# Performance work log

Hardware: AMD Instinct MI355X
Metric: run time of the kernel (lower is better)

Reference implementation:

```python
import jax, jax.numpy as jnp
import numpy as np
from jax import lax

B, T = 64, 200
NUM_C, DIM_S, SIZE_M = 2000, 128, 50


def setup_inputs() -> dict:
    key = jax.random.key(0)
    ks = jax.random.split(key, 12)
    d = {}
    d['skill'] = jax.random.randint(ks[0], (B, T), 0, NUM_C)
    d['answer'] = jax.random.randint(ks[1], (B, T), 0, 2)
    s = 1.0 / np.sqrt(DIM_S)
    d['k_emb'] = jax.random.normal(ks[2], (NUM_C + 1, DIM_S), jnp.float32)
    d['v_emb'] = jax.random.normal(ks[3], (2 * NUM_C + 1, DIM_S), jnp.float32)
    # kaiming_normal on [size_m, dim_s]: std = sqrt(2/dim_s)
    d['Mk'] = jax.random.normal(ks[4], (SIZE_M, DIM_S), jnp.float32) * np.sqrt(2.0 / DIM_S)
    d['Mv0'] = jax.random.normal(ks[5], (SIZE_M, DIM_S), jnp.float32) * np.sqrt(2.0 / DIM_S)
    d['f_W'] = jax.random.normal(ks[6], (DIM_S, 2 * DIM_S), jnp.float32) * (1.0 / np.sqrt(2 * DIM_S))
    d['f_b'] = jnp.zeros((DIM_S,), jnp.float32)
    d['p_W'] = jax.random.normal(ks[7], (NUM_C, DIM_S), jnp.float32) * s
    d['p_b'] = jnp.zeros((NUM_C,), jnp.float32)
    d['e_W'] = jax.random.normal(ks[8], (DIM_S, DIM_S), jnp.float32) * s
    d['e_b'] = jnp.zeros((DIM_S,), jnp.float32)
    d['a_W'] = jax.random.normal(ks[9], (DIM_S, DIM_S), jnp.float32) * s
    d['a_b'] = jnp.zeros((DIM_S,), jnp.float32)
    return d


def reference(skill, answer, k_emb, v_emb, Mk, Mv0, f_W, f_b, p_W, p_b, e_W, e_b, a_W, a_b):
    num_c = p_W.shape[0]
    bsz = skill.shape[0]
    answer_x = jnp.where(answer == 2, 1, answer)
    x = skill + num_c * answer_x                       # [B,T]
    k = k_emb[skill]                                   # [B,T,D]
    v = v_emb[x]                                       # [B,T,D]
    w = jax.nn.softmax(jnp.einsum('btd,md->btm', k, Mk), axis=-1)   # [B,T,M]
    e = jax.nn.sigmoid(jnp.einsum('btd,ed->bte', v, e_W) + e_b)      # [B,T,D]
    a = jnp.tanh(jnp.einsum('btd,ed->bte', v, a_W) + a_b)            # [B,T,D]

    Mv_init = jnp.broadcast_to(Mv0, (bsz,) + Mv0.shape)              # [B,M,D]

    def step(Mvt, inp):
        et, at, wt = inp                               # [B,D],[B,D],[B,M]
        # read uses pre-update memory (Mv[:, :-1] in the torch code)
        read = jnp.einsum('bm,bmd->bd', wt, Mvt)
        Mvt_new = Mvt * (1.0 - wt[:, :, None] * et[:, None, :]) + wt[:, :, None] * at[:, None, :]
        return Mvt_new, read

    _, reads = lax.scan(step, Mv_init,
                        (e.transpose(1, 0, 2), a.transpose(1, 0, 2), w.transpose(1, 0, 2)))
    reads = reads.transpose(1, 0, 2)                   # [B,T,D]

    f = jnp.tanh(jnp.concatenate([reads, k], axis=-1) @ f_W.T + f_b)  # [B,T,D]
    p = jax.nn.sigmoid(f @ p_W.T + p_b)                # [B,T,num_c] (dropout is identity at eval)
    p = p[:, :-1, :]
    next_skill = skill[:, 1:]                          # [B,T-1]
    idx = jnp.minimum(next_skill, num_c - 1)
    pred = jnp.take_along_axis(p, idx[..., None], axis=-1)[..., 0]
    pred = jnp.where(next_skill < num_c, pred, 0.0)    # index num_c -> zero row in torch one_hot
    return pred
```

## Files before the change

kernel.cpp:

```cpp
#include <hip/hip_runtime.h>
#include <math.h>

#define Bsz 64
#define Tn 200
#define NUMC 2000
#define DS 128
#define SM 50
#define NTOK (Bsz*Tn)

typedef __attribute__((ext_vector_type(8))) short bfrag;
typedef __attribute__((ext_vector_type(4))) float f32x4;
typedef __attribute__((ext_vector_type(4))) unsigned int u32x4;

__device__ __forceinline__ unsigned short f2bf(float x) {
    unsigned int u = __builtin_bit_cast(unsigned int, x);
    u = u + 0x7fffu + ((u >> 16) & 1u);
    return (unsigned short)(u >> 16);
}
__device__ __forceinline__ unsigned int pack2(float a, float b) {
    return (unsigned int)f2bf(a) | ((unsigned int)f2bf(b) << 16);
}
__device__ __forceinline__ bfrag mk_frag(f32x4 x, f32x4 y) {
    u32x4 t;
    t[0] = pack2(x[0], x[1]); t[1] = pack2(x[2], x[3]);
    t[2] = pack2(y[0], y[1]); t[3] = pack2(y[2], y[3]);
    return __builtin_bit_cast(bfrag, t);
}

__device__ __forceinline__ float fast_exp(float x)  { return __builtin_amdgcn_exp2f(x * 1.44269504f); }
__device__ __forceinline__ float fast_rcp(float x)  { return __builtin_amdgcn_rcpf(x); }
__device__ __forceinline__ float fast_sigmoid(float x) { return fast_rcp(1.f + fast_exp(-x)); }
__device__ __forceinline__ float fast_tanh(float x) { return 1.f - 2.f * fast_rcp(fast_exp(2.f * x) + 1.f); }

__global__ __launch_bounds__(256) void k0_cast(
    const float* __restrict__ eW, const float* __restrict__ aW,
    const float* __restrict__ fW, const float* __restrict__ Mk,
    unsigned int* __restrict__ BeaU, unsigned int* __restrict__ BkmU,
    unsigned int* __restrict__ Bf0U)
{
    const int g = blockIdx.x * 256 + threadIdx.x;
    if (g >= 9216) return;
    int gm, mat;
    unsigned int* dst;
    if (g < 4096)      { mat = 0; gm = g;        dst = BeaU; }
    else if (g < 7168) { mat = 1; gm = g - 4096; dst = BkmU; }
    else               { mat = 2; gm = g - 7168; dst = Bf0U; }
    const int nt = gm >> 8, r = gm & 255, ki = r >> 6, L = r & 63;
    const int n = nt * 16 + (L & 15);
    const int k = ki * 32 + (L >> 4) * 8;

    const float* src = nullptr;
    if (mat == 0) {
        src = (n < 128) ? (eW + (size_t)n * DS + k) : (aW + (size_t)(n - 128) * DS + k);
    } else if (mat == 1) {
        if (n < 128)      src = fW + (size_t)n * (2 * DS) + DS + k;
        else if (n < 128 + SM) src = Mk + (size_t)(n - 128) * DS + k;
    } else {
        src = fW + (size_t)n * (2 * DS) + k;
    }
    float v[8];
    #pragma unroll
    for (int j = 0; j < 8; j++) v[j] = src ? src[j] : 0.f;
    u32x4 o;
    o[0] = pack2(v[0], v[1]); o[1] = pack2(v[2], v[3]);
    o[2] = pack2(v[4], v[5]); o[3] = pack2(v[6], v[7]);
    ((u32x4*)dst)[gm] = o;
}

__global__ __launch_bounds__(64, 4) void k1_gemm(
    const int* __restrict__ skill, const int* __restrict__ answer,
    const float* __restrict__ k_emb, const float* __restrict__ v_emb,
    const unsigned int* __restrict__ BeaU, const unsigned int* __restrict__ BkmU,
    const float* __restrict__ eB, const float* __restrict__ aB,
    float* __restrict__ w2, float* __restrict__ e_buf,
    float* __restrict__ a_buf, float* __restrict__ kp_buf)
{
    const int bid = blockIdx.x;
    const int tile = bid / 7, role = bid % 7;
    const int L = threadIdx.x, L15 = L & 15, quad = L >> 4;
    const int tok0 = tile * 16;
    const int tokA = tok0 + L15;
    const int row0 = tok0 + quad * 4;

    const int s = skill[tokA];
    const float* ap;
    if (role < 4) {
        const int an = answer[tokA];
        const int ax = (an == 2) ? 1 : an;
        ap = v_emb + ((size_t)(s + NUMC * ax)) * DS + quad * 8;
    } else {
        ap = k_emb + (size_t)s * DS + quad * 8;
    }
    bfrag Af[4];
    #pragma unroll
    for (int ki = 0; ki < 4; ki++) {
        const f32x4* a4 = (const f32x4*)(ap + ki * 32);
        Af[ki] = mk_frag(a4[0], a4[1]);
    }

    const bfrag* Bp = (role < 4) ? (const bfrag*)BeaU : (const bfrag*)BkmU;
    const int g0 = (role < 4) ? role * 4 : (role - 4) * 4;

    f32x4 acc[4];
    #pragma unroll
    for (int t = 0; t < 4; t++) acc[t] = (f32x4){0.f,0.f,0.f,0.f};

    #pragma unroll
    for (int half = 0; half < 2; half++) {
        bfrag bh[2][4];
        #pragma unroll
        for (int tt = 0; tt < 2; tt++)
            #pragma unroll
            for (int ki = 0; ki < 4; ki++)
                bh[tt][ki] = Bp[(size_t)((g0 + half * 2 + tt) * 4 + ki) * 64 + L];
        #pragma unroll
        for (int ki = 0; ki < 4; ki++)
            #pragma unroll
            for (int tt = 0; tt < 2; tt++)
                acc[half * 2 + tt] = __builtin_amdgcn_mfma_f32_16x16x32_bf16(
                    Af[ki], bh[tt][ki], acc[half * 2 + tt], 0, 0, 0);
    }

    if (role == 6) {
        #pragma unroll
        for (int reg = 0; reg < 4; reg++) {
            float mx = -1e30f;
            #pragma unroll
            for (int t = 0; t < 4; t++) { const int c = t * 16 + L15; if (c < SM) mx = fmaxf(mx, acc[t][reg]); }
            #pragma unroll
            for (int msk = 1; msk <= 8; msk <<= 1) mx = fmaxf(mx, __shfl_xor(mx, msk));
            float ex[4]; float ssum = 0.f;
            #pragma unroll
            for (int t = 0; t < 4; t++) {
                const int c = t * 16 + L15;
                ex[t] = (c < SM) ? fast_exp(acc[t][reg] - mx) : 0.f;
                ssum += ex[t];
            }
            #pragma unroll
            for (int msk = 1; msk <= 8; msk <<= 1) ssum += __shfl_xor(ssum, msk);
            const float inv = fast_rcp(ssum);
            float* wp = w2 + (size_t)(row0 + reg) * 64;
            #pragma unroll
            for (int t = 0; t < 4; t++) {
                const int c = t * 16 + L15;
                const int idx = (c < 13) ? c
                              : (c < 26) ? c + 3
                              : (c < 39) ? c + 6
                              : (c < 50) ? c + 9
                              : (c < 53) ? c - 37
                              : (c < 56) ? c - 24
                              : (c < 59) ? c - 11
                              : c;
                wp[idx] = ex[t] * inv;
            }
        }
    } else {
        const int nb = (role & 1) * 64;
        float* obuf = (role < 2) ? e_buf : (role < 4) ? a_buf : kp_buf;
        const float* bias = (role < 2) ? eB : aB;
        #pragma unroll
        for (int t = 0; t < 4; t++) {
            const int n = nb + t * 16 + L15;
            const float bv = (role < 4) ? bias[n] : 0.f;
            #pragma unroll
            for (int reg = 0; reg < 4; reg++) {
                float v = acc[t][reg] + bv;
                if (role < 2)      v = fast_sigmoid(v);
                else if (role < 4) v = fast_tanh(v);
                obuf[(size_t)(row0 + reg) * DS + n] = v;
            }
        }
    }
}

__global__ __launch_bounds__(64) void k2_scan(
    const float* __restrict__ w2, const float* __restrict__ e_buf,
    const float* __restrict__ a_buf, const float* __restrict__ Mv0,
    unsigned short* __restrict__ reads)
{
    const int bid  = blockIdx.x;
    const int b    = bid >> 3;
    const int dseg = bid & 7;
    const int lane = threadIdx.x;
    const int mg   = lane >> 4;
    const int dd   = lane & 15;
    const int d    = dseg * 16 + dd;
    const int mstart = mg * 13;
    const int gcol = mg * 16;
    const int base = b * Tn;

    float Mv[13];
    #pragma unroll
    for (int j = 0; j < 13; j++) {
        const int m = (mstart + j < SM) ? (mstart + j) : (SM - 1);
        Mv[j] = Mv0[(size_t)m * DS + d];
    }

    float ev[2][4], av[2][4], wd[2][4];
    f32x4 wa[2][4], wb[2][4], wc[2][4];

    #define LOADS(S, T0)                                                       \
        { _Pragma("unroll")                                                    \
          for (int i_ = 0; i_ < 4; i_++) {                                     \
              const int t_ = (T0) + i_;                                        \
              const int tc_ = (t_ < Tn) ? t_ : 0;                              \
              ev[S][i_] = e_buf[(size_t)(base + tc_) * DS + d];                \
              av[S][i_] = a_buf[(size_t)(base + tc_) * DS + d];                \
              const float* wp_ = w2 + (size_t)(base + tc_) * 64 + gcol;        \
              wa[S][i_] = *(const f32x4*)wp_;                                  \
              wb[S][i_] = *(const f32x4*)(wp_ + 4);                            \
              wc[S][i_] = *(const f32x4*)(wp_ + 8);                            \
              wd[S][i_] = wp_[12];                                             \
          } }

    #define PROC4(S, T0)                                                       \
        { float r4[4];                                                         \
          _Pragma("unroll")                                                    \
          for (int it = 0; it < 4; it++) {                                     \
              const float ev_ = ev[S][it], av_ = av[S][it];                    \
              float rd = 0.f;                                                  \
              _Pragma("unroll")                                                \
              for (int j = 0; j < 13; j++) {                                   \
                  const float wm = (j < 4) ? wa[S][it][j]                      \
                                 : (j < 8) ? wb[S][it][j - 4]                  \
                                 : (j < 12) ? wc[S][it][j - 8]                 \
                                 : wd[S][it];                                  \
                  rd = fmaf(wm, Mv[j], rd);                        \
                  Mv[j] = fmaf(-wm, fmaf(ev_, Mv[j], -av_), Mv[j]);            \
              }                                                                \
              rd += __shfl_xor(rd, 16);                                        \
              rd += __shfl_xor(rd, 32);                                        \
              r4[it] = rd;                                                     \
          }                                                                    \
          const float val = (mg == 0) ? r4[0] : (mg == 1) ? r4[1]              \
                          : (mg == 2) ? r4[2] : r4[3];                         \
          reads[(size_t)(base + (T0) + mg) * DS + d] = f2bf(val); }

    LOADS(0, 0) LOADS(1, 4)

    for (int blk = 0; blk < 25; blk++) {
        const int t0 = blk * 8;
        PROC4(0, t0)     LOADS(0, t0 + 8)
        PROC4(1, t0 + 4) LOADS(1, t0 + 12)
    }
    #undef LOADS
    #undef PROC4
}

__global__ __launch_bounds__(128, 2) void k3_gemm(
    const unsigned short* __restrict__ reads, const float* __restrict__ kp_buf,
    const unsigned int* __restrict__ Bf0U, const float* __restrict__ fB,
    const float* __restrict__ pW, const float* __restrict__ pB,
    const int* __restrict__ skill, float* __restrict__ out)
{
    const int tid = threadIdx.x;
    const int wv  = tid >> 6;
    const int L   = tid & 63, L15 = L & 15, quad = L >> 4;
    const int tok0 = blockIdx.x * 16;
    const int tokA = tok0 + L15;
    const int row0 = tok0 + quad * 4;

    __shared__ float sm[2][16];

    bfrag Rf[4];
    #pragma unroll
    for (int ki = 0; ki < 4; ki++)
        Rf[ki] = *(const bfrag*)(reads + (size_t)tokA * DS + ki * 32 + quad * 8);

    const bfrag* Bf0 = (const bfrag*)Bf0U;
    const int g0 = wv * 4;

    f32x4 acc[4];
    #pragma unroll
    for (int t = 0; t < 4; t++) acc[t] = (f32x4){0.f,0.f,0.f,0.f};

    #pragma unroll
    for (int half = 0; half < 2; half++) {
        bfrag bh[2][4];
        #pragma unroll
        for (int tt = 0; tt < 2; tt++)
            #pragma unroll
            for (int ki = 0; ki < 4; ki++)
                bh[tt][ki] = Bf0[(size_t)((g0 + half * 2 + tt) * 4 + ki) * 64 + L];
        #pragma unroll
        for (int ki = 0; ki < 4; ki++)
            #pragma unroll
            for (int tt = 0; tt < 2; tt++)
                acc[half * 2 + tt] = __builtin_amdgcn_mfma_f32_16x16x32_bf16(
                    Rf[ki], bh[tt][ki], acc[half * 2 + tt], 0, 0, 0);
    }

    const int nb = wv * 64;
    float f[4][4];
    #pragma unroll
    for (int t = 0; t < 4; t++) {
        const int n = nb + t * 16 + L15;
        const float fb = fB[n];
        #pragma unroll
        for (int reg = 0; reg < 4; reg++)
            f[reg][t] = fast_tanh(acc[t][reg] + kp_buf[(size_t)(row0 + reg) * DS + n] + fb);
    }

    #pragma unroll
    for (int reg = 0; reg < 4; reg++) {
        const int tok = row0 + reg;
        const int t = tok % Tn;
        const bool act = (t < Tn - 1);
        float contrib = 0.f;
        if (act) {
            const int sn = skill[tok + 1];
            const int ix = (sn < NUMC) ? sn : (NUMC - 1);
            const float* pr = pW + (size_t)ix * DS + nb + L15;
            #pragma unroll
            for (int t4 = 0; t4 < 4; t4++)
                contrib = fmaf(f[reg][t4], pr[t4 * 16], contrib);
        }
        #pragma unroll
        for (int msk = 1; msk <= 8; msk <<= 1)
            contrib += __shfl_xor(contrib, msk);
        if (L15 == 0) sm[wv][quad * 4 + reg] = contrib;
    }
    __syncthreads();
    if (tid < 16) {
        const int tok = tok0 + tid;
        const int t = tok % Tn;
        if (t < Tn - 1) {
            const int sn = skill[tok + 1];
            const int ix = (sn < NUMC) ? sn : (NUMC - 1);
            const float val = sm[0][tid] + sm[1][tid] + pB[ix];
            out[(size_t)(tok / Tn) * (Tn - 1) + t] = (sn < NUMC) ? fast_sigmoid(val) : 0.f;
        }
    }
}

extern "C" void kernel_launch(void* const* d_in, const int* in_sizes, int n_in,
                              void* d_out, int out_size, void* d_ws, size_t ws_size,
                              hipStream_t stream)
{
    const int*   skill  = (const int*)  d_in[0];
    const int*   answer = (const int*)  d_in[1];
    const float* k_emb  = (const float*)d_in[2];
    const float* v_emb  = (const float*)d_in[3];
    const float* Mk     = (const float*)d_in[4];
    const float* Mv0    = (const float*)d_in[5];
    const float* f_W    = (const float*)d_in[6];
    const float* f_b    = (const float*)d_in[7];
    const float* p_W    = (const float*)d_in[8];
    const float* p_b    = (const float*)d_in[9];
    const float* e_W    = (const float*)d_in[10];
    const float* e_b    = (const float*)d_in[11];
    const float* a_W    = (const float*)d_in[12];
    const float* a_b    = (const float*)d_in[13];
    float* out = (float*)d_out;

    float* ws     = (float*)d_ws;
    float* w2     = ws;
    float* e_buf  = w2     + (size_t)NTOK*64;
    float* a_buf  = e_buf  + (size_t)NTOK*DS;
    float* kp_buf = a_buf  + (size_t)NTOK*DS;
    unsigned short* reads = (unsigned short*)(kp_buf + (size_t)NTOK*DS);
    unsigned int* BeaU = (unsigned int*)(reads + (size_t)NTOK*DS);
    unsigned int* BkmU = BeaU + 4096 * 4;
    unsigned int* Bf0U = BkmU + 3072 * 4;

    k0_cast<<<36, 256, 0, stream>>>(e_W, a_W, f_W, Mk, BeaU, BkmU, Bf0U);
    k1_gemm<<<7*(NTOK/16), 64, 0, stream>>>(skill, answer, k_emb, v_emb,
        BeaU, BkmU, e_b, a_b, w2, e_buf, a_buf, kp_buf);
    k2_scan<<<Bsz*8, 64, 0, stream>>>(w2, e_buf, a_buf, Mv0, reads);
    k3_gemm<<<NTOK/16, 128, 0, stream>>>(reads, kp_buf, Bf0U, f_b,
        p_W, p_b, skill, out);
}
```

Baseline: 137.5 us.

## Split scan across 32 blocks per batch with 4 memory slots per lane

The recurrent memory scan now gives each block 4 feature columns instead of 16. Each lane owns 4 memory slots instead of 13, which shortens the serial per-step dependency chain and launches four times as many blocks. The softmax weights are stored in their natural column order, zero-padded to 64, so each lane loads one float4 of weights per step. In exchange, each step needs two extra cross-lane shuffles for the read reduction, the weight rows are re-read by four times as many blocks, and the read stores are narrower.

New measurement: 134.2 us. 1.02x faster.

```diff
diff --git a/kernel.cpp b/kernel.cpp
--- a/kernel.cpp
+++ b/kernel.cpp
@@ -143,15 +143,7 @@
             #pragma unroll
             for (int t = 0; t < 4; t++) {
                 const int c = t * 16 + L15;
-                const int idx = (c < 13) ? c
-                              : (c < 26) ? c + 3
-                              : (c < 39) ? c + 6
-                              : (c < 50) ? c + 9
-                              : (c < 53) ? c - 37
-                              : (c < 56) ? c - 24
-                              : (c < 59) ? c - 11
-                              : c;
-                wp[idx] = ex[t] * inv;
+                wp[c] = ex[t] * inv;
             }
         }
     } else {
@@ -179,25 +171,24 @@
     unsigned short* __restrict__ reads)
 {
     const int bid  = blockIdx.x;
-    const int b    = bid >> 3;
-    const int dseg = bid & 7;
+    const int b    = bid >> 5;
+    const int dseg = bid & 31;
     const int lane = threadIdx.x;
-    const int mg   = lane >> 4;
-    const int dd   = lane & 15;
-    const int d    = dseg * 16 + dd;
-    const int mstart = mg * 13;
-    const int gcol = mg * 16;
+    const int mg   = lane >> 2;
+    const int dd   = lane & 3;
+    const int d    = dseg * 4 + dd;
+    const int m0   = mg * 4;
     const int base = b * Tn;
 
-    float Mv[13];
-    #pragma unroll
-    for (int j = 0; j < 13; j++) {
-        const int m = (mstart + j < SM) ? (mstart + j) : (SM - 1);
+    float Mv[4];
+    #pragma unroll
+    for (int j = 0; j < 4; j++) {
+        const int m = (m0 + j < SM) ? (m0 + j) : (SM - 1);
         Mv[j] = Mv0[(size_t)m * DS + d];
     }
 
-    float ev[2][4], av[2][4], wd[2][4];
-    f32x4 wa[2][4], wb[2][4], wc[2][4];
+    float ev[4][4], av[4][4];
+    f32x4 wv[4][4];
 
     #define LOADS(S, T0)                                                       \
         { _Pragma("unroll")                                                    \
@@ -206,11 +197,7 @@
               const int tc_ = (t_ < Tn) ? t_ : 0;                              \
               ev[S][i_] = e_buf[(size_t)(base + tc_) * DS + d];                \
               av[S][i_] = a_buf[(size_t)(base + tc_) * DS + d];                \
-              const float* wp_ = w2 + (size_t)(base + tc_) * 64 + gcol;        \
-              wa[S][i_] = *(const f32x4*)wp_;                                  \
-              wb[S][i_] = *(const f32x4*)(wp_ + 4);                            \
-              wc[S][i_] = *(const f32x4*)(wp_ + 8);                            \
-              wd[S][i_] = wp_[12];                                             \
+              wv[S][i_] = *(const f32x4*)(w2 + (size_t)(base + tc_) * 64 + m0);\
           } }
 
     #define PROC4(S, T0)                                                       \
@@ -220,29 +207,34 @@
               const float ev_ = ev[S][it], av_ = av[S][it];                    \
               float rd = 0.f;                                                  \
               _Pragma("unroll")                                                \
-              for (int j = 0; j < 13; j++) {                                   \
-                  const float wm = (j < 4) ? wa[S][it][j]                      \
-                                 : (j < 8) ? wb[S][it][j - 4]                  \
-                                 : (j < 12) ? wc[S][it][j - 8]                 \
-                                 : wd[S][it];                                  \
+              for (int j = 0; j < 4; j++) {                                    \
+                  const float wm = wv[S][it][j];                               \
                   rd = fmaf(wm, Mv[j], rd);                        \
                   Mv[j] = fmaf(-wm, fmaf(ev_, Mv[j], -av_), Mv[j]);            \
               }                                                                \
+              rd += __shfl_xor(rd, 4);                                         \
+              rd += __shfl_xor(rd, 8);                                         \
               rd += __shfl_xor(rd, 16);                                        \
               rd += __shfl_xor(rd, 32);                                        \
               r4[it] = rd;                                                     \
           }                                                                    \
-          const float val = (mg == 0) ? r4[0] : (mg == 1) ? r4[1]              \
-                          : (mg == 2) ? r4[2] : r4[3];                         \
-          reads[(size_t)(base + (T0) + mg) * DS + d] = f2bf(val); }
-
-    LOADS(0, 0) LOADS(1, 4)
-
-    for (int blk = 0; blk < 25; blk++) {
-        const int t0 = blk * 8;
-        PROC4(0, t0)     LOADS(0, t0 + 8)
-        PROC4(1, t0 + 4) LOADS(1, t0 + 12)
-    }
+          if (mg < 4) {                                                        \
+              const float val = (mg == 0) ? r4[0] : (mg == 1) ? r4[1]          \
+                              : (mg == 2) ? r4[2] : r4[3];                     \
+              reads[(size_t)(base + (T0) + mg) * DS + d] = f2bf(val);          \
+          } }
+
+    LOADS(0, 0) LOADS(1, 4) LOADS(2, 8) LOADS(3, 12)
+
+    for (int blk = 0; blk < 12; blk++) {
+        const int t0 = blk * 16;
+        PROC4(0, t0)      LOADS(0, t0 + 16)
+        PROC4(1, t0 + 4)  LOADS(1, t0 + 20)
+        PROC4(2, t0 + 8)  LOADS(2, t0 + 24)
+        PROC4(3, t0 + 12) LOADS(3, t0 + 28)
+    }
+    PROC4(0, 192)
+    PROC4(1, 196)
     #undef LOADS
     #undef PROC4
 }
@@ -366,7 +358,7 @@
     k0_cast<<<36, 256, 0, stream>>>(e_W, a_W, f_W, Mk, BeaU, BkmU, Bf0U);
     k1_gemm<<<7*(NTOK/16), 64, 0, stream>>>(skill, answer, k_emb, v_emb,
         BeaU, BkmU, e_b, a_b, w2, e_buf, a_buf, kp_buf);
-    k2_scan<<<Bsz*8, 64, 0, stream>>>(w2, e_buf, a_buf, Mv0, reads);
+    k2_scan<<<Bsz*32, 64, 0, stream>>>(w2, e_buf, a_buf, Mv0, reads);
     k3_gemm<<<NTOK/16, 128, 0, stream>>>(reads, kp_buf, Bf0U, f_b,
         p_W, p_b, skill, out);
 }
```
